# Kernel tuning notes

Hardware: AMD Instinct MI355X
Metric: run time of the kernel (lower is better)

The kernel has to match this reference:

```python
import jax, jax.numpy as jnp
import numpy as np

B, L, D1, D2 = 4, 2048, 1024, 1024

def setup_inputs() -> dict:
    key = jax.random.key(0)
    k1, k2, k3, k4, k5, k6 = jax.random.split(key, 6)
    s1 = 1.0 / np.sqrt(D1)
    s2 = 1.0 / np.sqrt(D2)
    return {
        "features_1": jax.random.normal(k1, (B, L, D1), dtype=jnp.float32),
        "features_2": jax.random.normal(k2, (B, L, D2), dtype=jnp.float32),
        # nn.Linear(d1, d2): W1 [d2, d1], b1 [d2]
        "W1": jax.random.uniform(k3, (D2, D1), jnp.float32, -s1, s1),
        "b1": jax.random.uniform(k4, (D2,), jnp.float32, -s1, s1),
        # nn.Linear(d2, d1): W2 [d1, d2], b2 [d1]
        "W2": jax.random.uniform(k5, (D1, D2), jnp.float32, -s2, s2),
        "b2": jax.random.uniform(k6, (D1,), jnp.float32, -s2, s2),
    }

def reference(features_1, features_2, W1, b1, W2, b2):
    # transformed_features_1: [B, L, D2]
    t1 = jnp.einsum('bld,ed->ble', features_1, W1) + b1
    # unscaled similarity: [B, L, L]
    sim = jnp.einsum('ble,bme->blm', t1, features_2)
    attn = jax.nn.softmax(sim, axis=-1)  # both softmaxes are identical
    attended_1 = jnp.einsum('blm,bme->ble', attn, features_2)  # [B, L, D2]
    attended_2 = jnp.einsum('blm,bme->ble', attn, t1)          # [B, L, D2]
    attended_2 = jnp.einsum('ble,de->bld', attended_2, W2) + b2  # [B, L, D1]
    return attended_1, attended_2
```

## Files before the change

kernel.cpp:

```cpp
#include <hip/hip_runtime.h>
#include <stdint.h>

#define BB 4
#define LL 2048
#define DD 1024

typedef __attribute__((ext_vector_type(4))) float f32x4;
typedef __attribute__((ext_vector_type(8))) _Float16 f16x8;
typedef __attribute__((ext_vector_type(4))) unsigned short u16x4;
typedef unsigned short u16;

__device__ __forceinline__ u16 f2h(float x){
  return __builtin_bit_cast(u16, (_Float16)x);
}

__device__ __forceinline__ void gload16(const u16* g, u16* l){
  __builtin_amdgcn_global_load_lds((const __attribute__((address_space(1))) unsigned*)g,
                                   (__attribute__((address_space(3))) unsigned*)l,
                                   16, 0, 0);
}

__device__ __forceinline__ int xcd_swz(int bx, int nwg){
  return (bx & 7) * (nwg >> 3) + (bx >> 3);
}

__device__ __forceinline__ void stage_tile8(u16* lds, const u16* src, int ld, int wave, int lane){
  const int r0 = lane >> 3;
  const int cs = (((lane & 7) ^ r0) << 3);
  #pragma unroll
  for (int j = 0; j < 2; ++j){
    const int rb = wave*16 + j*8;
    gload16(src + (size_t)(rb + r0)*ld + cs, lds + rb*64);
  }
}

__device__ __forceinline__ f16x8 frag_ld(const u16* t, int row, int ko){
  return __builtin_bit_cast(f16x8,
    *reinterpret_cast<const f32x4*>(t + row*64 + (ko ^ ((row & 7) << 3))));
}

__global__ void cast_k(const float* __restrict__ src, u16* __restrict__ dst, int n4){
  const int stride = gridDim.x * blockDim.x;
  for (int i = blockIdx.x*blockDim.x + threadIdx.x; i < n4; i += stride){
    f32x4 v = reinterpret_cast<const f32x4*>(src)[i];
    u16x4 h;
    #pragma unroll
    for (int j = 0; j < 4; ++j) h[j] = f2h(v[j]);
    reinterpret_cast<u16x4*>(dst)[i] = h;
  }
}

template<int EPI>
__global__ __launch_bounds__(512,4) void gemm_h_k(
    const u16* __restrict__ A_g, long long sAb, int lda,
    const u16* __restrict__ B_g, long long sBb, int ldb,
    float* __restrict__ C, long long sCb, int ldc,
    const float* __restrict__ bias, u16* __restrict__ Oh,
    int K, int tn_sh){
  __shared__ __align__(16) u16 As[128*64];
  __shared__ __align__(16) u16 Bs[128*64];
  const int b = blockIdx.y;
  const int bx = xcd_swz(blockIdx.x, gridDim.x);
  const int bm = bx >> tn_sh, bn = bx & ((1 << tn_sh) - 1);
  const int tid = threadIdx.x, wave = tid>>6, lane = tid&63;
  const int wr = wave>>2, wc = wave&3;
  const u16* Ab = A_g + (size_t)b*sAb + (size_t)(bm*128)*lda;
  const u16* Bb = B_g + (size_t)b*sBb + (size_t)(bn*128)*ldb;
  f32x4 acc[4][2];
  #pragma unroll
  for (int i=0;i<4;i++)
    #pragma unroll
    for (int j=0;j<2;j++) acc[i][j] = (f32x4){0.f,0.f,0.f,0.f};

  for (int k0 = 0; k0 < K; k0 += 64){
    __syncthreads();
    stage_tile8(As, Ab + k0, lda, wave, lane);
    stage_tile8(Bs, Bb + k0, ldb, wave, lane);
    __syncthreads();
    #pragma unroll
    for (int kk=0;kk<2;kk++){
      const int ko = kk*32 + ((lane>>4)<<3);
      f16x8 a[4], bb[2];
      #pragma unroll
      for (int mi=0;mi<4;mi++) a[mi]  = frag_ld(As, wr*64 + mi*16 + (lane&15), ko);
      #pragma unroll
      for (int ni=0;ni<2;ni++) bb[ni] = frag_ld(Bs, wc*32 + ni*16 + (lane&15), ko);
      #pragma unroll
      for (int mi=0;mi<4;mi++)
        #pragma unroll
        for (int ni=0;ni<2;ni++)
          acc[mi][ni] = __builtin_amdgcn_mfma_f32_16x16x32_f16(a[mi], bb[ni], acc[mi][ni], 0,0,0);
    }
  }
  const int m0 = bm*128, n0 = bn*128;
  if (EPI == 0){
    float* Cb = C + (size_t)b*sCb;
    #pragma unroll
    for (int mi=0;mi<4;mi++)
      #pragma unroll
      for (int ni=0;ni<2;ni++){
        const int r = m0 + wr*64 + mi*16 + ((lane>>4)<<2);
        const int c = n0 + wc*32 + ni*16 + (lane&15);
        #pragma unroll
        for (int j=0;j<4;j++)
          Cb[(size_t)(r+j)*ldc + c] = acc[mi][ni][j];
      }
  } else {
    #pragma unroll
    for (int mi=0;mi<4;mi++)
      #pragma unroll
      for (int ni=0;ni<2;ni++){
        const int r = m0 + wr*64 + mi*16 + ((lane>>4)<<2);
        const int c = n0 + wc*32 + ni*16 + (lane&15);
        const float bv = bias[c];
        #pragma unroll
        for (int j=0;j<4;j++)
          Oh[(size_t)(r+j)*ldc + c] = f2h(acc[mi][ni][j] + bv);
      }
  }
}

__global__ __launch_bounds__(256) void softmax_k(float* __restrict__ sim){
  const int row = blockIdx.x;
  float* p = sim + (size_t)row * LL;
  const int tid = threadIdx.x, wave = tid>>6, lane = tid&63;
  f32x4 x0 = reinterpret_cast<const f32x4*>(p)[tid];
  f32x4 x1 = reinterpret_cast<const f32x4*>(p)[tid + 256];
  float mx = fmaxf(fmaxf(fmaxf(x0[0],x0[1]), fmaxf(x0[2],x0[3])),
                   fmaxf(fmaxf(x1[0],x1[1]), fmaxf(x1[2],x1[3])));
  #pragma unroll
  for (int o = 32; o; o >>= 1) mx = fmaxf(mx, __shfl_xor(mx, o, 64));
  __shared__ float red[8];
  if (lane == 0) red[wave] = mx;
  __syncthreads();
  mx = fmaxf(fmaxf(red[0], red[1]), fmaxf(red[2], red[3]));
  float e0[4], e1[4], s = 0.f;
  #pragma unroll
  for (int j=0;j<4;j++){ e0[j] = __expf(x0[j]-mx); s += e0[j]; }
  #pragma unroll
  for (int j=0;j<4;j++){ e1[j] = __expf(x1[j]-mx); s += e1[j]; }
  #pragma unroll
  for (int o = 32; o; o >>= 1) s += __shfl_xor(s, o, 64);
  if (lane == 0) red[4+wave] = s;
  __syncthreads();
  s = (red[4]+red[5]) + (red[6]+red[7]);
  const float inv = 1.0f / s;
  u16* ob = reinterpret_cast<u16*>(p);
  u16x4 w0, w1;
  #pragma unroll
  for (int j=0;j<4;j++){ w0[j] = f2h(e0[j]*inv); w1[j] = f2h(e1[j]*inv); }
  reinterpret_cast<u16x4*>(ob)[tid]       = w0;
  reinterpret_cast<u16x4*>(ob)[tid + 256] = w1;
}

__global__ void transpose_k(const u16* __restrict__ in, u16* __restrict__ out){
  __shared__ u16 t[32][33];
  const int b = blockIdx.z;
  const int e0 = blockIdx.x*32, m0 = blockIdx.y*32;
  const u16* src = in  + (size_t)b*LL*DD;
  u16* dst       = out + (size_t)b*DD*LL;
  for (int j = threadIdx.y; j < 32; j += 8)
    t[j][threadIdx.x] = src[(size_t)(m0+j)*DD + e0 + threadIdx.x];
  __syncthreads();
  for (int j = threadIdx.y; j < 32; j += 8)
    dst[(size_t)(e0+j)*LL + m0 + threadIdx.x] = t[threadIdx.x][j];
}

__global__ __launch_bounds__(512,4) void gemm_zt_k(const u16* __restrict__ t1f,
                                                   const u16* __restrict__ w2f,
                                                   u16* __restrict__ ZT){
  __shared__ __align__(16) u16 As[128*64];
  __shared__ __align__(16) u16 Bs[128*64];
  const int bx = xcd_swz(blockIdx.x, gridDim.x);
  const int bm = bx >> 3, bn = bx & 7;
  const int tid = threadIdx.x, wave = tid>>6, lane = tid&63;
  const int wr = wave>>2, wc = wave&3;
  const u16* Ab = t1f + (size_t)(bm*128)*DD;
  const u16* Bb = w2f + (size_t)(bn*128)*DD;
  f32x4 acc[4][2];
  #pragma unroll
  for (int i=0;i<4;i++)
    #pragma unroll
    for (int j=0;j<2;j++) acc[i][j] = (f32x4){0.f,0.f,0.f,0.f};

  for (int k0 = 0; k0 < DD; k0 += 64){
    __syncthreads();
    stage_tile8(As, Ab + k0, DD, wave, lane);
    stage_tile8(Bs, Bb + k0, DD, wave, lane);
    __syncthreads();
    #pragma unroll
    for (int kk=0;kk<2;kk++){
      const int ko = kk*32 + ((lane>>4)<<3);
      f16x8 a[4], bb[2];
      #pragma unroll
      for (int mi=0;mi<4;mi++) a[mi]  = frag_ld(As, wr*64 + mi*16 + (lane&15), ko);
      #pragma unroll
      for (int ni=0;ni<2;ni++) bb[ni] = frag_ld(Bs, wc*32 + ni*16 + (lane&15), ko);
      #pragma unroll
      for (int mi=0;mi<4;mi++)
        #pragma unroll
        for (int ni=0;ni<2;ni++)
          acc[mi][ni] = __builtin_amdgcn_mfma_f32_16x16x32_f16(a[mi], bb[ni], acc[mi][ni], 0,0,0);
    }
  }
  #pragma unroll
  for (int mi=0;mi<4;mi++)
    #pragma unroll
    for (int ni=0;ni<2;ni++){
      const int l = bm*128 + wr*64 + mi*16 + ((lane>>4)<<2);
      const int b2i = l >> 11, m = l & 2047;
      const int d = bn*128 + wc*32 + ni*16 + (lane&15);
      u16x4 w;
      #pragma unroll
      for (int j=0;j<4;j++) w[j] = f2h(acc[mi][ni][j]);
      *reinterpret_cast<u16x4*>(ZT + ((size_t)b2i*DD + d)*LL + m) = w;
    }
}

__global__ __launch_bounds__(512,4) void gemm_pv_k(const u16* __restrict__ attn,
                                                   const u16* __restrict__ f2T,
                                                   const u16* __restrict__ ZT,
                                                   float* __restrict__ out1,
                                                   float* __restrict__ out2,
                                                   const float* __restrict__ b2){
  __shared__ __align__(16) u16 As[128*64];
  __shared__ __align__(16) u16 Bs[128*64];
  const int b = blockIdx.y;
  const int bx = xcd_swz(blockIdx.x, gridDim.x);
  const int bm = bx >> 4, bn = bx & 15;
  const int tid = threadIdx.x, wave = tid>>6, lane = tid&63;
  const int wr = wave>>2, wc = wave&3;
  const u16* Ab = attn + (size_t)b*LL*4096 + (size_t)(bm*128)*4096;
  const u16* Bbase = (bn < 8) ? f2T : ZT;
  const int d0 = (bn & 7) * 128;
  const u16* Bb = Bbase + (size_t)b*DD*LL + (size_t)d0*LL;
  f32x4 acc[4][2];
  #pragma unroll
  for (int i=0;i<4;i++)
    #pragma unroll
    for (int j=0;j<2;j++) acc[i][j] = (f32x4){0.f,0.f,0.f,0.f};

  for (int k0 = 0; k0 < LL; k0 += 64){
    __syncthreads();
    stage_tile8(As, Ab + k0, 4096, wave, lane);
    stage_tile8(Bs, Bb + k0, LL, wave, lane);
    __syncthreads();
    #pragma unroll
    for (int kk=0;kk<2;kk++){
      const int ko = kk*32 + ((lane>>4)<<3);
      f16x8 a[4], bb[2];
      #pragma unroll
      for (int mi=0;mi<4;mi++) a[mi]  = frag_ld(As, wr*64 + mi*16 + (lane&15), ko);
      #pragma unroll
      for (int ni=0;ni<2;ni++) bb[ni] = frag_ld(Bs, wc*32 + ni*16 + (lane&15), ko);
      #pragma unroll
      for (int mi=0;mi<4;mi++)
        #pragma unroll
        for (int ni=0;ni<2;ni++)
          acc[mi][ni] = __builtin_amdgcn_mfma_f32_16x16x32_f16(a[mi], bb[ni], acc[mi][ni], 0,0,0);
    }
  }
  float* O = ((bn < 8) ? out1 : out2) + (size_t)b*LL*DD;
  const bool has_bias = (bn >= 8);
  #pragma unroll
  for (int mi=0;mi<4;mi++)
    #pragma unroll
    for (int ni=0;ni<2;ni++){
      const int r = bm*128 + wr*64 + mi*16 + ((lane>>4)<<2);
      const int c = d0 + wc*32 + ni*16 + (lane&15);
      const float bv = has_bias ? b2[c] : 0.f;
      #pragma unroll
      for (int j=0;j<4;j++)
        O[(size_t)(r+j)*DD + c] = acc[mi][ni][j] + bv;
    }
}

extern "C" void kernel_launch(void* const* d_in, const int* in_sizes, int n_in,
                              void* d_out, int out_size, void* d_ws, size_t ws_size,
                              hipStream_t stream) {
  const float* f1 = (const float*)d_in[0];
  const float* f2 = (const float*)d_in[1];
  const float* W1 = (const float*)d_in[2];
  const float* b1 = (const float*)d_in[3];
  const float* W2 = (const float*)d_in[4];
  const float* b2 = (const float*)d_in[5];
  float* out1 = (float*)d_out;
  float* out2 = out1 + (size_t)BB*LL*DD;

  char* ws = (char*)d_ws;
  u16* t1f = (u16*)(ws + 0);
  u16* ZT  = (u16*)(ws + 16777216);
  u16* f2f = (u16*)(ws + 33554432);
  u16* f2T = (u16*)(ws + 50331648);
  u16* w1f = (u16*)(ws + 67108864);
  u16* w2f = (u16*)(ws + 69206016);
  float* sim = (float*)(ws + 71303168);
  u16* f1f = (u16*)(ws + 71303168);

  cast_k<<<4096, 256, 0, stream>>>(f2, f2f, (BB*LL*DD)/4);
  cast_k<<<4096, 256, 0, stream>>>(f1, f1f, (BB*LL*DD)/4);
  cast_k<<<1024, 256, 0, stream>>>(W1, w1f, (DD*DD)/4);
  cast_k<<<1024, 256, 0, stream>>>(W2, w2f, (DD*DD)/4);
  gemm_h_k<1><<<dim3(512, 1), 512, 0, stream>>>(f1f, 0, DD,
                                                w1f, 0, DD,
                                                nullptr, 0, DD,
                                                b1, t1f, DD, 3);
  gemm_h_k<0><<<dim3(256, BB), 512, 0, stream>>>(t1f, (long long)LL*DD, DD,
                                                 f2f, (long long)LL*DD, DD,
                                                 sim, (long long)LL*LL, LL,
                                                 nullptr, nullptr, DD, 4);
  softmax_k<<<BB*LL, 256, 0, stream>>>(sim);
  transpose_k<<<dim3(32, 64, BB), dim3(32, 8), 0, stream>>>(f2f, f2T);
  gemm_zt_k<<<dim3(512, 1), 512, 0, stream>>>(t1f, w2f, ZT);
  gemm_pv_k<<<dim3(256, BB), 512, 0, stream>>>((const u16*)sim, f2T, ZT,
                                               out1, out2, b2);
}
```

Baseline: 221.2 us.

## Use pipelined 256x256 GEMM kernel for similarity and attention-value products

Adds a new GEMM kernel with 256x256 output tiles split into four 128x128 quadrants, double-buffered LDS staging via async global-to-LDS loads, explicit vmcnt waits and s_setprio around MFMA bursts so loads overlap compute. It replaces both the QK similarity GEMM and the attention-times-(f2, Z) GEMM, cutting the grid to 64 blocks per batch. Larger tiles raise data reuse per block but use more registers and 128KB of LDS, lowering occupancy to two blocks, and leave fewer blocks to spread across CUs.

```diff
diff --git a/kernel.cpp b/kernel.cpp
--- a/kernel.cpp
+++ b/kernel.cpp
@@ -48,6 +48,121 @@
     for (int j = 0; j < 4; ++j) h[j] = f2h(v[j]);
     reinterpret_cast<u16x4*>(dst)[i] = h;
   }
+}
+
+template<int EPI>
+__global__ __launch_bounds__(512,2) void gemm8p_k(
+    const u16* __restrict__ A_g, long long sAb, int lda,
+    const u16* __restrict__ B0_g, const u16* __restrict__ B1_g, long long sBb, int ldb,
+    float* __restrict__ C0, float* __restrict__ C1, long long sCb, int ldc,
+    const float* __restrict__ bias, int NT){
+  __shared__ __align__(16) u16 As[4][128*64];
+  __shared__ __align__(16) u16 Bs[4][128*64];
+  const int b = blockIdx.y;
+  const int bx = xcd_swz(blockIdx.x, gridDim.x);
+  const int bm = bx >> 3, bn = bx & 7;
+  const int tid = threadIdx.x, wave = tid>>6, lane = tid&63;
+  const int wm = wave & 1, wn = wave >> 1;
+  const int r0 = lane >> 3, cs = (((lane&7) ^ r0) << 3);
+  const int rb0 = wave*16;
+  const u16* Ab = A_g + (size_t)b*sAb + (size_t)(bm*256)*lda;
+  const u16* Bb = (EPI == 0)
+      ? (B0_g + (size_t)b*sBb + (size_t)(bn*256)*ldb)
+      : (((bn < 4) ? B0_g : B1_g) + (size_t)b*sBb + (size_t)((bn&3)*256)*ldb);
+
+  f32x4 acc[2][2][4][2];
+  #pragma unroll
+  for (int i=0;i<2;i++)
+    #pragma unroll
+    for (int j=0;j<2;j++)
+      #pragma unroll
+      for (int m=0;m<4;m++)
+        #pragma unroll
+        for (int n=0;n<2;n++) acc[i][j][m][n] = (f32x4){0.f,0.f,0.f,0.f};
+
+  auto stA = [&](int tt, int h){
+    const u16* s = Ab + (size_t)(h*128 + rb0 + r0)*lda + (size_t)tt*64 + cs;
+    u16* d = &As[((tt&1)<<1)+h][rb0*64];
+    gload16(s, d);
+    gload16(s + (size_t)8*lda, d + 8*64);
+  };
+  auto stB = [&](int tt, int h){
+    const u16* s = Bb + (size_t)(h*128 + rb0 + r0)*ldb + (size_t)tt*64 + cs;
+    u16* d = &Bs[((tt&1)<<1)+h][rb0*64];
+    gload16(s, d);
+    gload16(s + (size_t)8*ldb, d + 8*64);
+  };
+
+  stA(0,0); stB(0,0); stA(0,1); stB(0,1);
+  stA(1,0); stB(1,0);
+  asm volatile("s_waitcnt vmcnt(4)" ::: "memory");
+  __builtin_amdgcn_s_barrier();
+
+  for (int t = 0; t < NT; ++t){
+    #pragma unroll
+    for (int p = 0; p < 4; ++p){
+      const u16* Ah = As[((t&1)<<1) + (p>>1)];
+      const u16* Bh = Bs[((t&1)<<1) + (p&1)];
+      f16x8 af[4][2], bf[2][2];
+      #pragma unroll
+      for (int mi=0;mi<4;mi++)
+        #pragma unroll
+        for (int ks=0;ks<2;ks++)
+          af[mi][ks] = frag_ld(Ah, wm*64 + mi*16 + (lane&15), ks*32 + ((lane>>4)<<3));
+      #pragma unroll
+      for (int ni=0;ni<2;ni++)
+        #pragma unroll
+        for (int ks=0;ks<2;ks++)
+          bf[ni][ks] = frag_ld(Bh, wn*32 + ni*16 + (lane&15), ks*32 + ((lane>>4)<<3));
+      if (p == 0){ if (t+1 < NT) stA(t+1, 1); }
+      else if (p == 1){ if (t+1 < NT) stB(t+1, 1); }
+      else if (p == 2){ if (t+2 < NT) stA(t+2, 0); }
+      else {
+        if (t+2 < NT){ stB(t+2, 0); asm volatile("s_waitcnt vmcnt(4)" ::: "memory"); }
+        else         {              asm volatile("s_waitcnt vmcnt(0)" ::: "memory"); }
+      }
+      __builtin_amdgcn_s_barrier();
+      asm volatile("s_waitcnt lgkmcnt(0)" ::: "memory");
+      __builtin_amdgcn_sched_barrier(0);
+      __builtin_amdgcn_s_setprio(1);
+      #pragma unroll
+      for (int mi=0;mi<4;mi++)
+        #pragma unroll
+        for (int ni=0;ni<2;ni++)
+          #pragma unroll
+          for (int ks=0;ks<2;ks++)
+            acc[p>>1][p&1][mi][ni] = __builtin_amdgcn_mfma_f32_16x16x32_f16(
+                af[mi][ks], bf[ni][ks], acc[p>>1][p&1][mi][ni], 0,0,0);
+      __builtin_amdgcn_s_setprio(0);
+      __builtin_amdgcn_sched_barrier(0);
+      __builtin_amdgcn_s_barrier();
+    }
+  }
+
+  #pragma unroll
+  for (int qm=0;qm<2;qm++)
+    #pragma unroll
+    for (int qn=0;qn<2;qn++)
+      #pragma unroll
+      for (int mi=0;mi<4;mi++)
+        #pragma unroll
+        for (int ni=0;ni<2;ni++){
+          const int r = bm*256 + qm*128 + wm*64 + mi*16 + ((lane>>4)<<2);
+          if (EPI == 0){
+            const int c = bn*256 + qn*128 + wn*32 + ni*16 + (lane&15);
+            float* Cb = C0 + (size_t)b*sCb;
+            #pragma unroll
+            for (int j=0;j<4;j++)
+              Cb[(size_t)(r+j)*ldc + c] = acc[qm][qn][mi][ni][j];
+          } else {
+            const int c = (bn&3)*256 + qn*128 + wn*32 + ni*16 + (lane&15);
+            float* O = ((bn < 4) ? C0 : C1) + (size_t)b*sCb;
+            const float bv = (bn >= 4) ? bias[c] : 0.f;
+            #pragma unroll
+            for (int j=0;j<4;j++)
+              O[(size_t)(r+j)*ldc + c] = acc[qm][qn][mi][ni][j] + bv;
+          }
+        }
 }
 
 template<int EPI>
@@ -217,64 +332,6 @@
     }
 }
 
-__global__ __launch_bounds__(512,4) void gemm_pv_k(const u16* __restrict__ attn,
-                                                   const u16* __restrict__ f2T,
-                                                   const u16* __restrict__ ZT,
-                                                   float* __restrict__ out1,
-                                                   float* __restrict__ out2,
-                                                   const float* __restrict__ b2){
-  __shared__ __align__(16) u16 As[128*64];
-  __shared__ __align__(16) u16 Bs[128*64];
-  const int b = blockIdx.y;
-  const int bx = xcd_swz(blockIdx.x, gridDim.x);
-  const int bm = bx >> 4, bn = bx & 15;
-  const int tid = threadIdx.x, wave = tid>>6, lane = tid&63;
-  const int wr = wave>>2, wc = wave&3;
-  const u16* Ab = attn + (size_t)b*LL*4096 + (size_t)(bm*128)*4096;
-  const u16* Bbase = (bn < 8) ? f2T : ZT;
-  const int d0 = (bn & 7) * 128;
-  const u16* Bb = Bbase + (size_t)b*DD*LL + (size_t)d0*LL;
-  f32x4 acc[4][2];
-  #pragma unroll
-  for (int i=0;i<4;i++)
-    #pragma unroll
-    for (int j=0;j<2;j++) acc[i][j] = (f32x4){0.f,0.f,0.f,0.f};
-
-  for (int k0 = 0; k0 < LL; k0 += 64){
-    __syncthreads();
-    stage_tile8(As, Ab + k0, 4096, wave, lane);
-    stage_tile8(Bs, Bb + k0, LL, wave, lane);
-    __syncthreads();
-    #pragma unroll
-    for (int kk=0;kk<2;kk++){
-      const int ko = kk*32 + ((lane>>4)<<3);
-      f16x8 a[4], bb[2];
-      #pragma unroll
-      for (int mi=0;mi<4;mi++) a[mi]  = frag_ld(As, wr*64 + mi*16 + (lane&15), ko);
-      #pragma unroll
-      for (int ni=0;ni<2;ni++) bb[ni] = frag_ld(Bs, wc*32 + ni*16 + (lane&15), ko);
-      #pragma unroll
-      for (int mi=0;mi<4;mi++)
-        #pragma unroll
-        for (int ni=0;ni<2;ni++)
-          acc[mi][ni] = __builtin_amdgcn_mfma_f32_16x16x32_f16(a[mi], bb[ni], acc[mi][ni], 0,0,0);
-    }
-  }
-  float* O = ((bn < 8) ? out1 : out2) + (size_t)b*LL*DD;
-  const bool has_bias = (bn >= 8);
-  #pragma unroll
-  for (int mi=0;mi<4;mi++)
-    #pragma unroll
-    for (int ni=0;ni<2;ni++){
-      const int r = bm*128 + wr*64 + mi*16 + ((lane>>4)<<2);
-      const int c = d0 + wc*32 + ni*16 + (lane&15);
-      const float bv = has_bias ? b2[c] : 0.f;
-      #pragma unroll
-      for (int j=0;j<4;j++)
-        O[(size_t)(r+j)*DD + c] = acc[mi][ni][j] + bv;
-    }
-}
-
 extern "C" void kernel_launch(void* const* d_in, const int* in_sizes, int n_in,
                               void* d_out, int out_size, void* d_ws, size_t ws_size,
                               hipStream_t stream) {
@@ -305,13 +362,15 @@
                                                 w1f, 0, DD,
                                                 nullptr, 0, DD,
                                                 b1, t1f, DD, 3);
-  gemm_h_k<0><<<dim3(256, BB), 512, 0, stream>>>(t1f, (long long)LL*DD, DD,
-                                                 f2f, (long long)LL*DD, DD,
-                                                 sim, (long long)LL*LL, LL,
-                                                 nullptr, nullptr, DD, 4);
+  gemm8p_k<0><<<dim3(64, BB), 512, 0, stream>>>(t1f, (long long)LL*DD, DD,
+                                                f2f, nullptr, (long long)LL*DD, DD,
+                                                sim, nullptr, (long long)LL*LL, LL,
+                                                nullptr, 16);
   softmax_k<<<BB*LL, 256, 0, stream>>>(sim);
   transpose_k<<<dim3(32, 64, BB), dim3(32, 8), 0, stream>>>(f2f, f2T);
   gemm_zt_k<<<dim3(512, 1), 512, 0, stream>>>(t1f, w2f, ZT);
-  gemm_pv_k<<<dim3(256, BB), 512, 0, stream>>>((const u16*)sim, f2T, ZT,
-                                               out1, out2, b2);
-}
+  gemm8p_k<1><<<dim3(64, BB), 512, 0, stream>>>((const u16*)sim, (long long)LL*4096, 4096,
+                                                f2T, ZT, (long long)DD*LL, LL,
+                                                out1, out2, (long long)LL*DD, DD,
+                                                b2, 32);
+}
```

Measured after the change: 213.8 us. 1.03x faster.
